# Kernel tuning notes

Measured on AMD Instinct MI355X. Metric: run time of the kernel, lower is better.

## Reference

```python
import jax, jax.numpy as jnp
import numpy as np

B, C, H, W, N = 32, 1280, 32, 32, 6890
HID, MID = 256, 128


def _grid_sample_bilinear(feat_map, verts_uv):
    """PyTorch F.grid_sample(mode='bilinear', padding_mode='zeros', align_corners=True)
    for a (B,N,1,2) grid, returning (B,N,C).
    feat_map: (B,C,H,W); verts_uv: (B,N,2) with (x,y) in [-1,1]."""
    Bc, Cc, Hc, Wc = feat_map.shape
    # unnormalize with align_corners=True
    x = (verts_uv[..., 0] + 1.0) * 0.5 * (Wc - 1)  # (B,N)
    y = (verts_uv[..., 1] + 1.0) * 0.5 * (Hc - 1)
    x0 = jnp.floor(x); y0 = jnp.floor(y)
    wx = x - x0; wy = y - y0
    x0i = x0.astype(jnp.int32); y0i = y0.astype(jnp.int32)
    x1i = x0i + 1; y1i = y0i + 1

    feat_flat = feat_map.reshape(Bc, Cc, Hc * Wc)

    def gather(yi, xi):
        valid = (xi >= 0) & (xi < Wc) & (yi >= 0) & (yi < Hc)  # zeros padding
        idx = jnp.clip(yi, 0, Hc - 1) * Wc + jnp.clip(xi, 0, Wc - 1)  # (B,N)
        g = jnp.take_along_axis(feat_flat, idx[:, None, :], axis=2)  # (B,C,N)
        return g, valid.astype(feat_map.dtype)

    g00, m00 = gather(y0i, x0i)
    g01, m01 = gather(y0i, x1i)
    g10, m10 = gather(y1i, x0i)
    g11, m11 = gather(y1i, x1i)

    w00 = ((1.0 - wy) * (1.0 - wx) * m00)[:, None, :]
    w01 = ((1.0 - wy) * wx * m01)[:, None, :]
    w10 = (wy * (1.0 - wx) * m10)[:, None, :]
    w11 = (wy * wx * m11)[:, None, :]

    out = g00 * w00 + g01 * w01 + g10 * w10 + g11 * w11  # (B,C,N)
    return jnp.transpose(out, (0, 2, 1))  # (B,N,C)


def setup_inputs() -> dict:
    key = jax.random.key(0)
    ks = jax.random.split(key, 8)
    feat_map = jax.random.normal(ks[0], (B, C, H, W), dtype=jnp.float32)
    verts_uv = jax.random.uniform(ks[1], (B, N, 2), dtype=jnp.float32, minval=-1.0, maxval=1.0)
    reduce_w = jax.random.normal(ks[2], (C, HID), dtype=jnp.float32) * (1.0 / np.sqrt(C))
    reduce_b = jax.random.normal(ks[3], (HID,), dtype=jnp.float32) * 0.02
    cls_w1 = jax.random.normal(ks[4], (HID, MID), dtype=jnp.float32) * (1.0 / np.sqrt(HID))
    cls_b1 = jax.random.normal(ks[5], (MID,), dtype=jnp.float32) * 0.02
    cls_w2 = jax.random.normal(ks[6], (MID,), dtype=jnp.float32) * (1.0 / np.sqrt(MID))
    cls_b2 = jax.random.normal(ks[7], (1,), dtype=jnp.float32) * 0.02
    return {"feat_map": feat_map, "verts_uv": verts_uv, "reduce_w": reduce_w,
            "reduce_b": reduce_b, "cls_w1": cls_w1, "cls_b1": cls_b1,
            "cls_w2": cls_w2, "cls_b2": cls_b2}


def reference(feat_map, verts_uv, reduce_w, reduce_b, cls_w1, cls_b1, cls_w2, cls_b2):
    v_feat = _grid_sample_bilinear(feat_map, verts_uv)          # (B,N,C)
    v_feat = jnp.einsum('bnc,cd->bnd', v_feat, reduce_w) + reduce_b  # (B,N,HID)
    h = jax.nn.relu(jnp.einsum('bnd,dm->bnm', v_feat, cls_w1) + cls_b1)  # (B,N,MID)
    logits = jnp.einsum('bnm,m->bn', h, cls_w2) + cls_b2[0]     # (B,N)
    return jax.nn.sigmoid(logits)
```

## Files before the change

### kernel.cpp

```cpp
#include <hip/hip_runtime.h>
#include <hip/hip_bf16.h>
#include <math.h>

#define B_    32
#define C_    1280
#define H_    32
#define W_    32
#define N_    6890
#define HID_  256
#define MID_  128
#define HW_   (H_ * W_)
#define KSTEP 32
#define KITER (C_ / KSTEP)

typedef __attribute__((ext_vector_type(8))) short short8v;
typedef __attribute__((ext_vector_type(4))) float f32x4;

__global__ __launch_bounds__(256) void k_wcomb(
        const float* __restrict__ rw, const float* __restrict__ w1,
        const float* __restrict__ b1, const float* __restrict__ rb,
        __hip_bfloat16* __restrict__ bpack, float* __restrict__ bcomb) {
    if (blockIdx.x == (C_ * MID_) / 256) {
        int m = threadIdx.x;
        if (m < MID_) {
            float acc = b1[m];
            for (int d = 0; d < HID_; ++d)
                acc = fmaf(rb[d], w1[d * MID_ + m], acc);
            bcomb[m] = acc;
        }
        return;
    }
    int o = blockIdx.x * 256 + threadIdx.x;
    int c = o >> 7, m = o & 127;
    const float* rwc = rw + (size_t)c * HID_;
    float acc = 0.f;
#pragma unroll 8
    for (int d = 0; d < HID_; ++d)
        acc = fmaf(rwc[d], w1[d * MID_ + m], acc);

    int ks = c >> 5, kr = c & 31;
    int lh = kr >> 3, ii = kr & 7;
    int nb = m >> 4, col = m & 15;
    size_t idx = ((size_t)((ks * 8 + nb) * 64 + lh * 16 + col)) * 8 + ii;
    bpack[idx] = __float2bfloat16(acc);
}

__global__ __launch_bounds__(256) void k_pregemm(
        const float* __restrict__ feat,
        const __hip_bfloat16* __restrict__ bpack,
        float* __restrict__ fred) {
    const int b  = blockIdx.y;
    const int p0 = blockIdx.x * 64;
    const float* F = feat + (size_t)b * C_ * HW_ + p0;

    __shared__ __align__(16) float As[64][36];

    const int t  = threadIdx.x;
    const int wv = t >> 6;
    const int l  = t & 63;

    const int c_loc  = 16 * (wv & 1) + (l & 15);
    const int p_loc0 = 16 * (wv >> 1) + 4 * (l >> 4);
    const int p_loc1 = p_loc0 + 32;

    const int arow = l & 15;
    const int akb  = 8 * (l >> 4);

    f32x4 acc[4][2];
#pragma unroll
    for (int mi = 0; mi < 4; ++mi)
#pragma unroll
        for (int nb = 0; nb < 2; ++nb) acc[mi][nb] = (f32x4)0.f;

    const short8v* Bp = (const short8v*)bpack;

    float4 r0 = *(const float4*)&F[(size_t)c_loc * HW_ + p_loc0];
    float4 r1 = *(const float4*)&F[(size_t)c_loc * HW_ + p_loc1];

    for (int s = 0; s < KITER; ++s) {
        __syncthreads();
        {
            const float* q0 = (const float*)&r0;
            const float* q1 = (const float*)&r1;
#pragma unroll
            for (int j = 0; j < 4; ++j) As[p_loc0 + j][c_loc] = q0[j];
#pragma unroll
            for (int j = 0; j < 4; ++j) As[p_loc1 + j][c_loc] = q1[j];
        }
        __syncthreads();

        if (s + 1 < KITER) {
            const float* Fn = F + (size_t)(s + 1) * KSTEP * HW_;
            r0 = *(const float4*)&Fn[(size_t)c_loc * HW_ + p_loc0];
            r1 = *(const float4*)&Fn[(size_t)c_loc * HW_ + p_loc1];
        }

        short8v bfr0 = Bp[(size_t)(s * 8 + wv * 2 + 0) * 64 + l];
        short8v bfr1 = Bp[(size_t)(s * 8 + wv * 2 + 1) * 64 + l];

        short8v afr[4];
#pragma unroll
        for (int mi = 0; mi < 4; ++mi) {
            const float* ap = &As[16 * mi + arow][akb];
            float4 lo = *(const float4*)ap;
            float4 hi = *(const float4*)(ap + 4);
            union { short8v v; __hip_bfloat16 h[8]; } u;
            const float* lp = (const float*)&lo;
            const float* hp = (const float*)&hi;
#pragma unroll
            for (int i2 = 0; i2 < 4; ++i2) u.h[i2]     = __float2bfloat16(lp[i2]);
#pragma unroll
            for (int i2 = 0; i2 < 4; ++i2) u.h[4 + i2] = __float2bfloat16(hp[i2]);
            afr[mi] = u.v;
        }

#pragma unroll
        for (int mi = 0; mi < 4; ++mi) {
            acc[mi][0] = __builtin_amdgcn_mfma_f32_16x16x32_bf16(afr[mi], bfr0, acc[mi][0], 0, 0, 0);
            acc[mi][1] = __builtin_amdgcn_mfma_f32_16x16x32_bf16(afr[mi], bfr1, acc[mi][1], 0, 0, 0);
        }
    }

    float* Ob = fred + ((size_t)b * HW_ + p0) * MID_;
    const int rbase = 4 * (l >> 4);
    const int ncol0 = 32 * wv + (l & 15);
#pragma unroll
    for (int mi = 0; mi < 4; ++mi)
#pragma unroll
        for (int nb = 0; nb < 2; ++nb)
#pragma unroll
            for (int i = 0; i < 4; ++i) {
                int prow = 16 * mi + rbase + i;
                Ob[(size_t)prow * MID_ + ncol0 + 16 * nb] = acc[mi][nb][i];
            }
}

__global__ __launch_bounds__(256) void k_sample_head(const float* __restrict__ verts,
                                                     const float* __restrict__ fred,
                                                     const float* __restrict__ bcomb,
                                                     const float* __restrict__ w2,
                                                     const float* __restrict__ b2,
                                                     float* __restrict__ out) {
    const int wave = (blockIdx.x * 256 + threadIdx.x) >> 6;
    const int lane = threadIdx.x & 63;
    if (wave >= B_ * N_) return;
    const int b = wave / N_;
    const int n = wave - b * N_;

    const float u = verts[((size_t)b * N_ + n) * 2 + 0];
    const float v = verts[((size_t)b * N_ + n) * 2 + 1];
    const float x = (u + 1.f) * 0.5f * (float)(W_ - 1);
    const float y = (v + 1.f) * 0.5f * (float)(H_ - 1);
    const float x0f = floorf(x), y0f = floorf(y);
    const float wx = x - x0f, wy = y - y0f;
    const int x0 = (int)x0f, y0 = (int)y0f;
    const int x1 = x0 + 1,   y1 = y0 + 1;

    const float mx0 = (x0 >= 0 && x0 < W_) ? 1.f : 0.f;
    const float mx1 = (x1 >= 0 && x1 < W_) ? 1.f : 0.f;
    const float my0 = (y0 >= 0 && y0 < H_) ? 1.f : 0.f;
    const float my1 = (y1 >= 0 && y1 < H_) ? 1.f : 0.f;

    const int cx0 = min(max(x0, 0), W_ - 1), cx1 = min(max(x1, 0), W_ - 1);
    const int cy0 = min(max(y0, 0), H_ - 1), cy1 = min(max(y1, 0), H_ - 1);

    const float w00 = (1.f - wy) * (1.f - wx) * my0 * mx0;
    const float w01 = (1.f - wy) * wx         * my0 * mx1;
    const float w10 = wy         * (1.f - wx) * my1 * mx0;
    const float w11 = wy         * wx         * my1 * mx1;

    const float* Fb = fred + (size_t)b * HW_ * MID_;
    const float2 a00 = ((const float2*)&Fb[(size_t)(cy0 * W_ + cx0) * MID_])[lane];
    const float2 a01 = ((const float2*)&Fb[(size_t)(cy0 * W_ + cx1) * MID_])[lane];
    const float2 a10 = ((const float2*)&Fb[(size_t)(cy1 * W_ + cx0) * MID_])[lane];
    const float2 a11 = ((const float2*)&Fb[(size_t)(cy1 * W_ + cx1) * MID_])[lane];

    const float2 bc  = ((const float2*)bcomb)[lane];
    const float2 w2v = ((const float2*)w2)[lane];

    float hx = a00.x * w00 + a01.x * w01 + a10.x * w10 + a11.x * w11 + bc.x;
    float hy = a00.y * w00 + a01.y * w01 + a10.y * w10 + a11.y * w11 + bc.y;
    hx = fmaxf(hx, 0.f);
    hy = fmaxf(hy, 0.f);

    float s = hx * w2v.x + hy * w2v.y;
#pragma unroll
    for (int off = 32; off >= 1; off >>= 1)
        s += __shfl_xor(s, off);

    if (lane == 0) {
        const float logit = s + b2[0];
        out[wave] = 1.f / (1.f + expf(-logit));
    }
}

extern "C" void kernel_launch(void* const* d_in, const int* in_sizes, int n_in,
                              void* d_out, int out_size, void* d_ws, size_t ws_size,
                              hipStream_t stream) {
    const float* feat  = (const float*)d_in[0];
    const float* verts = (const float*)d_in[1];
    const float* rw    = (const float*)d_in[2];
    const float* rb    = (const float*)d_in[3];
    const float* w1    = (const float*)d_in[4];
    const float* b1    = (const float*)d_in[5];
    const float* w2    = (const float*)d_in[6];
    const float* b2    = (const float*)d_in[7];
    float* out = (float*)d_out;

    float* ws = (float*)d_ws;
    float* fred = ws;
    __hip_bfloat16* bpack = (__hip_bfloat16*)(fred + (size_t)B_ * HW_ * MID_);
    float* bcomb = (float*)(bpack + (size_t)C_ * MID_);

    k_wcomb<<<(C_ * MID_) / 256 + 1, 256, 0, stream>>>(rw, w1, b1, rb, bpack, bcomb);

    dim3 g2(HW_ / 64, B_);
    k_pregemm<<<g2, 256, 0, stream>>>(feat, bpack, fred);

    const int nwave = B_ * N_;
    k_sample_head<<<(nwave + 3) / 4, 256, 0, stream>>>(verts, fred, bcomb, w2, b2, out);
}
```

Baseline: 318.6 us.

## Store intermediate features in bf16, double-buffer swizzled LDS, and remap sample blocks

```diff
diff --git a/kernel.cpp b/kernel.cpp
--- a/kernel.cpp
+++ b/kernel.cpp
@@ -12,9 +12,17 @@
 #define HW_   (H_ * W_)
 #define KSTEP 32
 #define KITER (C_ / KSTEP)
+#define LSTR  20
 
 typedef __attribute__((ext_vector_type(8))) short short8v;
 typedef __attribute__((ext_vector_type(4))) float f32x4;
+
+static __device__ __forceinline__ uint pkbf(float a, float b) {
+    union { __hip_bfloat16 h; ushort u; } ua, ub;
+    ua.h = __float2bfloat16(a);
+    ub.h = __float2bfloat16(b);
+    return (uint)ua.u | ((uint)ub.u << 16);
+}
 
 __global__ __launch_bounds__(256) void k_wcomb(
         const float* __restrict__ rw, const float* __restrict__ w1,
@@ -48,23 +56,26 @@
 __global__ __launch_bounds__(256) void k_pregemm(
         const float* __restrict__ feat,
         const __hip_bfloat16* __restrict__ bpack,
-        float* __restrict__ fred) {
+        __hip_bfloat16* __restrict__ fredh) {
     const int b  = blockIdx.y;
     const int p0 = blockIdx.x * 64;
     const float* F = feat + (size_t)b * C_ * HW_ + p0;
 
-    __shared__ __align__(16) float As[64][36];
+    __shared__ uint As[2][64][LSTR];
 
     const int t  = threadIdx.x;
     const int wv = t >> 6;
     const int l  = t & 63;
 
-    const int c_loc  = 16 * (wv & 1) + (l & 15);
-    const int p_loc0 = 16 * (wv >> 1) + 4 * (l >> 4);
-    const int p_loc1 = p_loc0 + 32;
+    const int pl   = l & 7;
+    const int ql   = l >> 3;
+    const int pair = (wv & 1) * 8 + ql;
+    const int px0  = 4 * pl + 32 * (wv >> 1);
+    const int wcol = pair ^ ((((px0 >> 3) & 1) << 3) | (((px0 >> 4) & 1) << 2));
 
     const int arow = l & 15;
-    const int akb  = 8 * (l >> 4);
+    const int g    = l >> 4;
+    const int crd  = (4 * g) ^ (((arow >> 3) & 1) << 3);
 
     f32x4 acc[4][2];
 #pragma unroll
@@ -74,54 +85,41 @@
 
     const short8v* Bp = (const short8v*)bpack;
 
-    float4 r0 = *(const float4*)&F[(size_t)c_loc * HW_ + p_loc0];
-    float4 r1 = *(const float4*)&F[(size_t)c_loc * HW_ + p_loc1];
+    float4 r0 = *(const float4*)&F[(size_t)(2 * pair + 0) * HW_ + px0];
+    float4 r1 = *(const float4*)&F[(size_t)(2 * pair + 1) * HW_ + px0];
+    short8v b0c = Bp[(size_t)(0 * 8 + wv * 2 + 0) * 64 + l];
+    short8v b1c = Bp[(size_t)(0 * 8 + wv * 2 + 1) * 64 + l];
 
     for (int s = 0; s < KITER; ++s) {
-        __syncthreads();
+        const int buf = s & 1;
         {
             const float* q0 = (const float*)&r0;
             const float* q1 = (const float*)&r1;
 #pragma unroll
-            for (int j = 0; j < 4; ++j) As[p_loc0 + j][c_loc] = q0[j];
-#pragma unroll
-            for (int j = 0; j < 4; ++j) As[p_loc1 + j][c_loc] = q1[j];
+            for (int j = 0; j < 4; ++j)
+                As[buf][px0 + j][wcol] = pkbf(q0[j], q1[j]);
         }
         __syncthreads();
 
+        short8v b0n = b0c, b1n = b1c;
         if (s + 1 < KITER) {
             const float* Fn = F + (size_t)(s + 1) * KSTEP * HW_;
-            r0 = *(const float4*)&Fn[(size_t)c_loc * HW_ + p_loc0];
-            r1 = *(const float4*)&Fn[(size_t)c_loc * HW_ + p_loc1];
-        }
-
-        short8v bfr0 = Bp[(size_t)(s * 8 + wv * 2 + 0) * 64 + l];
-        short8v bfr1 = Bp[(size_t)(s * 8 + wv * 2 + 1) * 64 + l];
-
-        short8v afr[4];
+            r0 = *(const float4*)&Fn[(size_t)(2 * pair + 0) * HW_ + px0];
+            r1 = *(const float4*)&Fn[(size_t)(2 * pair + 1) * HW_ + px0];
+            b0n = Bp[(size_t)((s + 1) * 8 + wv * 2 + 0) * 64 + l];
+            b1n = Bp[(size_t)((s + 1) * 8 + wv * 2 + 1) * 64 + l];
+        }
+
 #pragma unroll
         for (int mi = 0; mi < 4; ++mi) {
-            const float* ap = &As[16 * mi + arow][akb];
-            float4 lo = *(const float4*)ap;
-            float4 hi = *(const float4*)(ap + 4);
-            union { short8v v; __hip_bfloat16 h[8]; } u;
-            const float* lp = (const float*)&lo;
-            const float* hp = (const float*)&hi;
-#pragma unroll
-            for (int i2 = 0; i2 < 4; ++i2) u.h[i2]     = __float2bfloat16(lp[i2]);
-#pragma unroll
-            for (int i2 = 0; i2 < 4; ++i2) u.h[4 + i2] = __float2bfloat16(hp[i2]);
-            afr[mi] = u.v;
-        }
-
-#pragma unroll
-        for (int mi = 0; mi < 4; ++mi) {
-            acc[mi][0] = __builtin_amdgcn_mfma_f32_16x16x32_bf16(afr[mi], bfr0, acc[mi][0], 0, 0, 0);
-            acc[mi][1] = __builtin_amdgcn_mfma_f32_16x16x32_bf16(afr[mi], bfr1, acc[mi][1], 0, 0, 0);
-        }
+            short8v afr = *(const short8v*)&As[buf][16 * mi + arow][crd ^ ((mi & 1) << 2)];
+            acc[mi][0] = __builtin_amdgcn_mfma_f32_16x16x32_bf16(afr, b0c, acc[mi][0], 0, 0, 0);
+            acc[mi][1] = __builtin_amdgcn_mfma_f32_16x16x32_bf16(afr, b1c, acc[mi][1], 0, 0, 0);
+        }
+        b0c = b0n; b1c = b1n;
     }
 
-    float* Ob = fred + ((size_t)b * HW_ + p0) * MID_;
+    __hip_bfloat16* Ob = fredh + ((size_t)b * HW_ + p0) * MID_;
     const int rbase = 4 * (l >> 4);
     const int ncol0 = 32 * wv + (l & 15);
 #pragma unroll
@@ -131,17 +129,18 @@
 #pragma unroll
             for (int i = 0; i < 4; ++i) {
                 int prow = 16 * mi + rbase + i;
-                Ob[(size_t)prow * MID_ + ncol0 + 16 * nb] = acc[mi][nb][i];
+                Ob[(size_t)prow * MID_ + ncol0 + 16 * nb] = __float2bfloat16(acc[mi][nb][i]);
             }
 }
 
 __global__ __launch_bounds__(256) void k_sample_head(const float* __restrict__ verts,
-                                                     const float* __restrict__ fred,
+                                                     const uint* __restrict__ fredu,
                                                      const float* __restrict__ bcomb,
                                                      const float* __restrict__ w2,
                                                      const float* __restrict__ b2,
                                                      float* __restrict__ out) {
-    const int wave = (blockIdx.x * 256 + threadIdx.x) >> 6;
+    const int bid  = (blockIdx.x & 7) * (B_ * N_ / 4 / 8) + (blockIdx.x >> 3);
+    const int wave = (bid * 256 + (int)threadIdx.x) >> 6;
     const int lane = threadIdx.x & 63;
     if (wave >= B_ * N_) return;
     const int b = wave / N_;
@@ -169,17 +168,22 @@
     const float w10 = wy         * (1.f - wx) * my1 * mx0;
     const float w11 = wy         * wx         * my1 * mx1;
 
-    const float* Fb = fred + (size_t)b * HW_ * MID_;
-    const float2 a00 = ((const float2*)&Fb[(size_t)(cy0 * W_ + cx0) * MID_])[lane];
-    const float2 a01 = ((const float2*)&Fb[(size_t)(cy0 * W_ + cx1) * MID_])[lane];
-    const float2 a10 = ((const float2*)&Fb[(size_t)(cy1 * W_ + cx0) * MID_])[lane];
-    const float2 a11 = ((const float2*)&Fb[(size_t)(cy1 * W_ + cx1) * MID_])[lane];
+    const uint* Fb = fredu + (size_t)b * HW_ * (MID_ / 2);
+    const uint u00 = Fb[(size_t)(cy0 * W_ + cx0) * (MID_ / 2) + lane];
+    const uint u01 = Fb[(size_t)(cy0 * W_ + cx1) * (MID_ / 2) + lane];
+    const uint u10 = Fb[(size_t)(cy1 * W_ + cx0) * (MID_ / 2) + lane];
+    const uint u11 = Fb[(size_t)(cy1 * W_ + cx1) * (MID_ / 2) + lane];
 
     const float2 bc  = ((const float2*)bcomb)[lane];
     const float2 w2v = ((const float2*)w2)[lane];
 
-    float hx = a00.x * w00 + a01.x * w01 + a10.x * w10 + a11.x * w11 + bc.x;
-    float hy = a00.y * w00 + a01.y * w01 + a10.y * w10 + a11.y * w11 + bc.y;
+    const float lo00 = __uint_as_float(u00 << 16), hi00 = __uint_as_float(u00 & 0xffff0000u);
+    const float lo01 = __uint_as_float(u01 << 16), hi01 = __uint_as_float(u01 & 0xffff0000u);
+    const float lo10 = __uint_as_float(u10 << 16), hi10 = __uint_as_float(u10 & 0xffff0000u);
+    const float lo11 = __uint_as_float(u11 << 16), hi11 = __uint_as_float(u11 & 0xffff0000u);
+
+    float hx = lo00 * w00 + lo01 * w01 + lo10 * w10 + lo11 * w11 + bc.x;
+    float hy = hi00 * w00 + hi01 * w01 + hi10 * w10 + hi11 * w11 + bc.y;
     hx = fmaxf(hx, 0.f);
     hy = fmaxf(hy, 0.f);
 
@@ -207,16 +211,15 @@
     const float* b2    = (const float*)d_in[7];
     float* out = (float*)d_out;
 
-    float* ws = (float*)d_ws;
-    float* fred = ws;
-    __hip_bfloat16* bpack = (__hip_bfloat16*)(fred + (size_t)B_ * HW_ * MID_);
-    float* bcomb = (float*)(bpack + (size_t)C_ * MID_);
+    __hip_bfloat16* fredh = (__hip_bfloat16*)d_ws;
+    __hip_bfloat16* bpack = fredh + (size_t)B_ * HW_ * MID_;
+    float*          bcomb = (float*)(bpack + (size_t)C_ * MID_);
 
     k_wcomb<<<(C_ * MID_) / 256 + 1, 256, 0, stream>>>(rw, w1, b1, rb, bpack, bcomb);
 
     dim3 g2(HW_ / 64, B_);
-    k_pregemm<<<g2, 256, 0, stream>>>(feat, bpack, fred);
-
-    const int nwave = B_ * N_;
-    k_sample_head<<<(nwave + 3) / 4, 256, 0, stream>>>(verts, fred, bcomb, w2, b2, out);
-}
+    k_pregemm<<<g2, 256, 0, stream>>>(feat, bpack, fredh);
+
+    const int nblk = B_ * N_ / 4;
+    k_sample_head<<<nblk, 256, 0, stream>>>(verts, (const uint*)fredh, bcomb, w2, b2, out);
+}
```

Result: faster. 308.4 us (-3.2%).
